# Kernel optimization log

Measured on AMD Instinct MI355X. Metric: run time of the kernel, lower is better.

The kernel has to match this reference:

```python
import jax, jax.numpy as jnp
import numpy as np

B, S, DM, H = 2, 2048, 1024, 16        # dim_model = d_model//2 = 1024
WINDOW, DILATION, N_GLOBAL = 513, 2, 32
HD = DM // H
NEG = -1e9


def build_mask(n, window_size, dilation, global_idx):
    # dilated local window: |i-j| <= (window//2)*dilation and (i-j) % dilation == 0
    i = jnp.arange(n)[:, None]
    j = jnp.arange(n)[None, :]
    d = j - i
    half = window_size // 2
    local = (jnp.abs(d) <= half * dilation) & (jnp.mod(d, dilation) == 0)
    g = jnp.zeros((n,), bool).at[global_idx].set(True)
    # symmetric global token mask: global rows and columns fully attend
    return local | g[:, None] | g[None, :]


def setup_inputs() -> dict:
    key = jax.random.key(0)
    ks = jax.random.split(key, 9)
    std = 0.02
    inp = {
        "q": jax.random.normal(ks[0], (B, S, DM), jnp.float32),
        "k": jax.random.normal(ks[1], (B, S, DM), jnp.float32),
        "v": jax.random.normal(ks[2], (B, S, DM), jnp.float32),
        "Wq": jax.random.normal(ks[3], (DM, DM), jnp.float32) * std,
        "Wk": jax.random.normal(ks[4], (DM, DM), jnp.float32) * std,
        "Wv": jax.random.normal(ks[5], (DM, DM), jnp.float32) * std,
        "Wo": jax.random.normal(ks[6], (DM, DM), jnp.float32) * std,
        "bq": jnp.zeros((DM,), jnp.float32),
        "bk": jnp.zeros((DM,), jnp.float32),
        "bv": jnp.zeros((DM,), jnp.float32),
        "bo": jnp.zeros((DM,), jnp.float32),
        "global_idx": jax.random.randint(ks[7], (N_GLOBAL,), 0, S, jnp.int64)
        if jax.config.jax_enable_x64 else jax.random.randint(ks[7], (N_GLOBAL,), 0, S, jnp.int32),
    }
    return inp


def reference(q, k, v, Wq, Wk, Wv, Wo, bq, bk, bv, bo, global_idx):
    def split(x):  # [B,S,DM] -> [B,H,S,HD]
        return x.reshape(B, S, H, HD).transpose(0, 2, 1, 3)

    qh = split(q @ Wq.T + bq)
    kh = split(k @ Wk.T + bk)
    vh = split(v @ Wv.T + bv)

    scores = jnp.einsum("bhqd,bhkd->bhqk", qh, kh) / jnp.sqrt(jnp.asarray(HD, qh.dtype))
    mask = build_mask(S, WINDOW, DILATION, global_idx)  # [S,S] bool
    scores = jnp.where(mask[None, None], scores, NEG)
    attn = jax.nn.softmax(scores, axis=-1)
    out = jnp.einsum("bhqk,bhkd->bhqd", attn, vh)
    out = out.transpose(0, 2, 1, 3).reshape(B, S, DM)
    return out @ Wo.T + bo
```

## Files before the change

kernel.cpp:

```cpp
#include <hip/hip_runtime.h>
#include <hip/hip_bf16.h>
#include <math.h>

#define BB 2
#define SS 2048
#define DMM 1024
#define HH 16
#define HDD 64
#define NGLOB 32
#define MM 4096
#define SCALE2 0.18033688f

typedef __attribute__((ext_vector_type(8))) short short8;
typedef __attribute__((ext_vector_type(4))) float float4v;

__device__ __forceinline__ short f2bf(float f) {
    union { float f; unsigned u; } x; x.f = f;
    unsigned r = (x.u + 0x7fffu + ((x.u >> 16) & 1u)) >> 16;
    return (short)r;
}

#define ASYNC16(gp, lp) __builtin_amdgcn_global_load_lds( \
    (__attribute__((address_space(1))) void*)(gp), \
    (__attribute__((address_space(3))) void*)(lp), 16, 0, 0)

#define VSL(dim, key) ((dim) * 40 + (((((key) >> 3) ^ (((dim) >> 3) & 3)) << 3) | ((key) & 7)))

__global__ __launch_bounds__(256)
void convert_flat(const float* __restrict__ q, const float* __restrict__ k,
                  const float* __restrict__ v,
                  const float* __restrict__ w0, const float* __restrict__ w1,
                  const float* __restrict__ w2, const float* __restrict__ w3,
                  short* __restrict__ abf, short* __restrict__ wbf,
                  const int* __restrict__ gidx, int* __restrict__ g,
                  int* __restrict__ glist, int* __restrict__ gcount,
                  int* __restrict__ bcnt) {
    int bid = blockIdx.x;
    int t = threadIdx.x;
    if (bid == 6144 + 2048) {
        for (int i = t; i < SS; i += 256) g[i] = 0;
        if (t == 0) *gcount = 0;
        if (t < 32) bcnt[t] = 0;
        __syncthreads();
        if (t < NGLOB) {
            int j = gidx[t];
            if (j >= 0 && j < SS) g[j] = 1;
        }
        __syncthreads();
        for (int j = t; j < SS; j += 256) {
            if (g[j]) {
                int p = atomicAdd(gcount, 1);
                glist[p] = j;
            }
        }
        return;
    }
    const float* src;
    short* dst;
    if (bid < 6144) {
        int z = bid >> 11;
        size_t off = ((size_t)(bid & 2047) << 11) + (size_t)t * 8;
        src = ((z == 0) ? q : (z == 1) ? k : v) + off;
        dst = abf + ((size_t)z << 22) + off;
    } else {
        int y = (bid - 6144) >> 9;
        size_t off = ((size_t)((bid - 6144) & 511) << 11) + (size_t)t * 8;
        src = ((y == 0) ? w0 : (y == 1) ? w1 : (y == 2) ? w2 : w3) + off;
        dst = wbf + ((size_t)y << 20) + off;
    }
    float4 a = *(const float4*)(src);
    float4 b = *(const float4*)(src + 4);
    short8 s;
    s[0]=f2bf(a.x); s[1]=f2bf(a.y); s[2]=f2bf(a.z); s[3]=f2bf(a.w);
    s[4]=f2bf(b.x); s[5]=f2bf(b.y); s[6]=f2bf(b.z); s[7]=f2bf(b.w);
    *(short8*)dst = s;
}

template<int OBF, int HEADSPLIT>
__global__ __launch_bounds__(512, 2)
void gemm256(const short* __restrict__ Abase, const short* __restrict__ Wbase,
             const float* __restrict__ b0, const float* __restrict__ b1,
             const float* __restrict__ b2,
             void* __restrict__ O0p, void* __restrict__ O1p, void* __restrict__ O2p) {
    __shared__ short As[2][256 * 64];
    __shared__ short Ws[2][256 * 64];

    int t = threadIdx.x;
    int z = blockIdx.y;
    const short* A    = Abase + (size_t)z * ((size_t)MM * DMM);
    const short* W    = Wbase + (size_t)z * ((size_t)DMM * DMM);
    const float* bias = (z == 0) ? b0 : (z == 1) ? b1 : b2;
    void* outp        = (z == 0) ? O0p : (z == 1) ? O1p : O2p;

    int bid = blockIdx.x;
    int mt = bid & 15, nt = bid >> 4;
    int m0 = mt * 256, n0 = nt * 256;

    int lane = t & 63, w = t >> 6;
    int quad = lane >> 4, col = lane & 15;
    int wm = (w >> 2) * 128;
    int wn = (w & 3) * 64;

    float4v acc[8][4];
    #pragma unroll
    for (int i = 0; i < 8; i++)
        #pragma unroll
        for (int j = 0; j < 4; j++) acc[i][j] = (float4v){0, 0, 0, 0};

    int srow = t >> 3;
    int scol = ((t & 7) ^ (srow & 7)) * 8;
    const short* Ap = A + (size_t)(m0 + srow) * DMM + scol;
    const short* Wp = W + (size_t)(n0 + srow) * DMM + scol;

    #define ST_W(bf, tt, h) ASYNC16(Wp + (size_t)(h) * 64 * DMM + (size_t)(tt) * 64, \
                                    &Ws[bf][(h) * 4096 + t * 8])
    #define ST_A(bf, tt, h) ASYNC16(Ap + (size_t)(h) * 64 * DMM + (size_t)(tt) * 64, \
                                    &As[bf][(h) * 4096 + t * 8])

    int c7 = col & 7;

    ST_W(0, 0, 0); ST_W(0, 0, 1); ST_W(0, 0, 2); ST_W(0, 0, 3);
    ST_A(0, 0, 0); ST_A(0, 0, 2); ST_A(0, 0, 1); ST_A(0, 0, 3);
    asm volatile("s_waitcnt vmcnt(2)" ::: "memory");
    __builtin_amdgcn_s_barrier();

    for (int it = 0; it < 16; it++) {
        int cur = it & 1, nb = cur ^ 1;
        bool pf = (it < 15);

        short8 bF[4][2];
        #pragma unroll
        for (int j = 0; j < 4; j++) {
            int rB = (wn + 16 * j + col) * 64;
            #pragma unroll
            for (int ks = 0; ks < 2; ks++)
                bF[j][ks] = *(short8*)&Ws[cur][rB + ((((ks << 2) | quad) ^ c7) << 3)];
        }

        #pragma unroll
        for (int p = 0; p < 4; p++) {
            short8 aF[2][2];
            #pragma unroll
            for (int u = 0; u < 2; u++) {
                int rA = (wm + 16 * (2 * p + u) + col) * 64;
                #pragma unroll
                for (int ks = 0; ks < 2; ks++)
                    aF[u][ks] = *(short8*)&As[cur][rA + ((((ks << 2) | quad) ^ c7) << 3)];
            }
            if (pf) {
                if (p == 0)      { ST_W(nb, it + 1, 0); ST_W(nb, it + 1, 1); }
                else if (p == 1) { ST_W(nb, it + 1, 2); ST_W(nb, it + 1, 3); }
                else if (p == 2) { ST_A(nb, it + 1, 0); ST_A(nb, it + 1, 2); }
                else             { ST_A(nb, it + 1, 1); ST_A(nb, it + 1, 3); }
            }
            __builtin_amdgcn_s_barrier();
            __builtin_amdgcn_s_setprio(1);
            #pragma unroll
            for (int ks = 0; ks < 2; ks++)
                #pragma unroll
                for (int u = 0; u < 2; u++)
                    #pragma unroll
                    for (int j = 0; j < 4; j++)
                        acc[2 * p + u][j] = __builtin_amdgcn_mfma_f32_16x16x32_bf16(
                            aF[u][ks], bF[j][ks], acc[2 * p + u][j], 0, 0, 0);
            __builtin_amdgcn_s_setprio(0);
            if (p == 1) {
                if (pf) asm volatile("s_waitcnt vmcnt(4)" ::: "memory");
                else    asm volatile("s_waitcnt vmcnt(0)" ::: "memory");
            }
            if (p == 3 && pf)
                asm volatile("s_waitcnt vmcnt(2)" ::: "memory");
            __builtin_amdgcn_s_barrier();
        }
    }
    #undef ST_W
    #undef ST_A

    #pragma unroll
    for (int i = 0; i < 8; i++) {
        #pragma unroll
        for (int j = 0; j < 4; j++) {
            int n = n0 + wn + 16 * j + col;
            float bn = bias[n];
            #pragma unroll
            for (int r = 0; r < 4; r++) {
                int m = m0 + wm + 16 * i + quad * 4 + r;
                float val = acc[i][j][r] + bn;
                size_t idx;
                if (HEADSPLIT) {
                    int b = m >> 11;
                    int s = m & 2047;
                    int h = n >> 6;
                    int hd = n & 63;
                    idx = (((size_t)b * HH + h) * SS + s) * HDD + hd;
                } else {
                    idx = (size_t)m * DMM + n;
                }
                if (OBF) ((short*)outp)[idx] = f2bf(val);
                else     ((float*)outp)[idx] = val;
            }
        }
    }
}

__global__ __launch_bounds__(512, 2)
void gemm128wo(const short* __restrict__ A, const short* __restrict__ W,
               const float* __restrict__ bias, float* __restrict__ out) {
    __shared__ short As[2][128 * 64];
    __shared__ short Ws[2][128 * 64];

    int t = threadIdx.x;
    int bid = blockIdx.x;
    int mt = bid & 31, nt = bid >> 5;
    int m0 = mt * 128, n0 = nt * 128;

    int lane = t & 63, w = t >> 6;
    int quad = lane >> 4, col = lane & 15;
    int wm = (w >> 2) * 64;
    int wn = (w & 3) * 32;

    float4v acc[4][2];
    #pragma unroll
    for (int i = 0; i < 4; i++)
        #pragma unroll
        for (int j = 0; j < 2; j++) acc[i][j] = (float4v){0, 0, 0, 0};

    int srow = t >> 3;
    int scol = ((t & 7) ^ (srow & 7)) * 8;
    const short* Ap = A + (size_t)(m0 + srow) * DMM + scol;
    const short* Wp = W + (size_t)(n0 + srow) * DMM + scol;

    #define STAGEWO(bf, tt) do { size_t kk = (size_t)(tt) * 64; \
        ASYNC16(Ap + kk,                      &As[bf][t * 8]); \
        ASYNC16(Ap + 64 * (size_t)DMM + kk,   &As[bf][4096 + t * 8]); \
        ASYNC16(Wp + kk,                      &Ws[bf][t * 8]); \
        ASYNC16(Wp + 64 * (size_t)DMM + kk,   &Ws[bf][4096 + t * 8]); \
    } while (0)

    int c7 = col & 7;

    STAGEWO(0, 0);

    for (int it = 0; it < 16; it++) {
        int cur = it & 1;
        if (it < 15) {
            STAGEWO(cur ^ 1, it + 1);
            asm volatile("s_waitcnt vmcnt(4)" ::: "memory");
        } else {
            asm volatile("s_waitcnt vmcnt(0)" ::: "memory");
        }
        __builtin_amdgcn_s_barrier();

        short8 bF[2][2];
        #pragma unroll
        for (int j = 0; j < 2; j++) {
            int rB = (wn + 16 * j + col) * 64;
            #pragma unroll
            for (int ks = 0; ks < 2; ks++)
                bF[j][ks] = *(short8*)&Ws[cur][rB + ((((ks << 2) | quad) ^ c7) << 3)];
        }

        #pragma unroll
        for (int p = 0; p < 2; p++) {
            if (p) __builtin_amdgcn_s_barrier();
            short8 aF[2][2];
            #pragma unroll
            for (int u = 0; u < 2; u++) {
                int rA = (wm + 16 * (2 * p + u) + col) * 64;
                #pragma unroll
                for (int ks = 0; ks < 2; ks++)
                    aF[u][ks] = *(short8*)&As[cur][rA + ((((ks << 2) | quad) ^ c7) << 3)];
            }
            __builtin_amdgcn_s_setprio(1);
            #pragma unroll
            for (int ks = 0; ks < 2; ks++)
                #pragma unroll
                for (int u = 0; u < 2; u++)
                    #pragma unroll
                    for (int j = 0; j < 2; j++)
                        acc[2 * p + u][j] = __builtin_amdgcn_mfma_f32_16x16x32_bf16(
                            aF[u][ks], bF[j][ks], acc[2 * p + u][j], 0, 0, 0);
            __builtin_amdgcn_s_setprio(0);
        }
        __builtin_amdgcn_s_barrier();
    }
    #undef STAGEWO

    #pragma unroll
    for (int i = 0; i < 4; i++) {
        #pragma unroll
        for (int j = 0; j < 2; j++) {
            int n = n0 + wn + 16 * j + col;
            float bn = bias[n];
            #pragma unroll
            for (int r = 0; r < 4; r++) {
                int m = m0 + wm + 16 * i + quad * 4 + r;
                out[(size_t)m * DMM + n] = acc[i][j][r] + bn;
            }
        }
    }
}

__global__ __launch_bounds__(256)
void attn_fused(const short* __restrict__ qh, const short* __restrict__ kh,
                const short* __restrict__ vh, const int* __restrict__ glist,
                const int* __restrict__ gcount, const int* __restrict__ gmap,
                short* __restrict__ ao, float* __restrict__ pl, float* __restrict__ pO,
                int* __restrict__ bcnt) {
    __shared__ __align__(16) char smem[29200];
    int t = threadIdx.x;
    int bid = blockIdx.x;
    int nG = *gcount;

    if (bid < 1024) {
        short* Qs = (short*)smem;
        short* Ks = Qs + 64 * 72;
        short* Vt = Ks + 32 * 72;
        short* Ps = Vt + 64 * 40;
        int*   gjs = (int*)(Ps + 4 * 16 * 40);

        int xcd = bid & 7, idx = bid >> 3;
        int gl  = idx >> 4;
        int qt  = idx & 15;
        int gid = xcd * 8 + gl;
        int z   = gid >> 4;
        int h   = gid & 15;
        int b = z >> 1, p = z & 1;
        int qq0 = qt * 64;

        const short* Qb = qh + ((size_t)(b * HH + h) * SS) * HDD;
        const short* Kb = kh + ((size_t)(b * HH + h) * SS) * HDD;
        const short* Vb = vh + ((size_t)(b * HH + h) * SS) * HDD;

        int row8 = t >> 3;
        int dim8 = (t & 7) * 8;

        #pragma unroll
        for (int rr = 0; rr < 2; rr++) {
            int row = rr * 32 + row8;
            int i = 2 * (qq0 + row) + p;
            short8 qv = *(const short8*)(Qb + (size_t)i * HDD + dim8);
            *(short8*)&Qs[row * 72 + dim8] = qv;
        }
        if (t < 32) gjs[t] = (t < nG) ? glist[t] : -1000000;
        __syncthreads();

        int lane = t & 63, w = t >> 6;
        int quad = lane >> 4, col = lane & 15;

        short8 qf0 = *(short8*)&Qs[(16 * w + col) * 72 + quad * 8];
        short8 qf1 = *(short8*)&Qs[(16 * w + col) * 72 + 32 + quad * 8];

        float4v O0 = {0,0,0,0}, O1 = {0,0,0,0}, O2 = {0,0,0,0}, O3 = {0,0,0,0};
        float lst[4] = {0.f, 0.f, 0.f, 0.f};

        short8 kvP, vvP, kvN, vvN;
        {
            int srow = 2 * (qq0 - 256 + row8) + p;
            srow = srow < 0 ? 0 : (srow > SS - 1 ? SS - 1 : srow);
            kvP = *(const short8*)(Kb + (size_t)srow * HDD + dim8);
            vvP = *(const short8*)(Vb + (size_t)srow * HDD + dim8);
        }

        for (int c = 0; c < 19; c++) {
            __syncthreads();
            *(short8*)&Ks[row8 * 72 + dim8] = kvP;
            #pragma unroll
            for (int j = 0; j < 8; j++) {
                int d = dim8 + j;
                Vt[VSL(d, row8)] = vvP[j];
            }
            if (c < 18) {
                int cn = c + 1;
                int ch0n = qq0 - 256 + cn * 32;
                int srow;
                if (cn < 18) srow = 2 * (ch0n + row8) + p;
                else         srow = (row8 < nG) ? gjs[row8] : 0;
                srow = srow < 0 ? 0 : (srow > SS - 1 ? SS - 1 : srow);
                kvN = *(const short8*)(Kb + (size_t)srow * HDD + dim8);
                vvN = *(const short8*)(Vb + (size_t)srow * HDD + dim8);
            }
            __syncthreads();

            int ch0 = qq0 - 256 + c * 32;

            short8 kA0 = *(short8*)&Ks[col * 72 + quad * 8];
            short8 kA1 = *(short8*)&Ks[col * 72 + 32 + quad * 8];
            short8 kB0 = *(short8*)&Ks[(16 + col) * 72 + quad * 8];
            short8 kB1 = *(short8*)&Ks[(16 + col) * 72 + 32 + quad * 8];
            float4v sA = {0,0,0,0}, sB = {0,0,0,0};
            sA = __builtin_amdgcn_mfma_f32_16x16x32_bf16(qf0, kA0, sA, 0, 0, 0);
            sA = __builtin_amdgcn_mfma_f32_16x16x32_bf16(qf1, kA1, sA, 0, 0, 0);
            sB = __builtin_amdgcn_mfma_f32_16x16x32_bf16(qf0, kB0, sB, 0, 0, 0);
            sB = __builtin_amdgcn_mfma_f32_16x16x32_bf16(qf1, kB1, sB, 0, 0, 0);

            if (c < 18) {
                int nlo = -ch0;
                int nhi = 1023 - ch0;
                #pragma unroll
                for (int r = 0; r < 4; r++) {
                    int qq = qq0 + 16 * w + quad * 4 + r;
                    int u  = qq - ch0;
                    int lo = max(u - 256, nlo);
                    int hi = min(u + 256, nhi);
                    bool vA = (col >= lo) && (col <= hi);
                    bool vB = (col + 16 >= lo) && (col + 16 <= hi);
                    float pa = vA ? exp2f(sA[r] * SCALE2) : 0.f;
                    float pb = vB ? exp2f(sB[r] * SCALE2) : 0.f;
                    lst[r] += pa + pb;
                    Ps[(w * 16 + quad * 4 + r) * 40 + col]      = f2bf(pa);
                    Ps[(w * 16 + quad * 4 + r) * 40 + col + 16] = f2bf(pb);
                }
            } else {
                #pragma unroll
                for (int r = 0; r < 4; r++) {
                    int qq = qq0 + 16 * w + quad * 4 + r;
                    int i = 2 * qq + p;
                    int jA = gjs[col], jB = gjs[col + 16];
                    int dA = jA - i, dB = jB - i;
                    int aA = dA < 0 ? -dA : dA;
                    int aB = dB < 0 ? -dB : dB;
                    bool vA = (jA >= 0) && !((aA <= 512) && ((dA & 1) == 0));
                    bool vB = (jB >= 0) && !((aB <= 512) && ((dB & 1) == 0));
                    float pa = vA ? exp2f(sA[r] * SCALE2) : 0.f;
                    float pb = vB ? exp2f(sB[r] * SCALE2) : 0.f;
                    lst[r] += pa + pb;
                    Ps[(w * 16 + quad * 4 + r) * 40 + col]      = f2bf(pa);
                    Ps[(w * 16 + quad * 4 + r) * 40 + col + 16] = f2bf(pb);
                }
            }
            asm volatile("s_waitcnt lgkmcnt(0)" ::: "memory");

            short8 pf  = *(short8*)&Ps[(w * 16 + col) * 40 + quad * 8];
            short8 vf0 = *(short8*)&Vt[(col) * 40 + ((quad ^ ((col >> 3) & 3)) << 3)];
            short8 vf1 = *(short8*)&Vt[(16 + col) * 40 + ((quad ^ (((16 + col) >> 3) & 3)) << 3)];
            short8 vf2 = *(short8*)&Vt[(32 + col) * 40 + ((quad ^ (((32 + col) >> 3) & 3)) << 3)];
            short8 vf3 = *(short8*)&Vt[(48 + col) * 40 + ((quad ^ (((48 + col) >> 3) & 3)) << 3)];
            O0 = __builtin_amdgcn_mfma_f32_16x16x32_bf16(pf, vf0, O0, 0, 0, 0);
            O1 = __builtin_amdgcn_mfma_f32_16x16x32_bf16(pf, vf1, O1, 0, 0, 0);
            O2 = __builtin_amdgcn_mfma_f32_16x16x32_bf16(pf, vf2, O2, 0, 0, 0);
            O3 = __builtin_amdgcn_mfma_f32_16x16x32_bf16(pf, vf3, O3, 0, 0, 0);

            kvP = kvN; vvP = vvN;
        }

        #pragma unroll
        for (int r = 0; r < 4; r++) {
            float l = lst[r];
            #pragma unroll
            for (int mk = 1; mk < 16; mk <<= 1) l += __shfl_xor(l, mk);
            float inv = 1.0f / l;
            int q = 16 * w + quad * 4 + r;
            int i = 2 * (qq0 + q) + p;
            if (!gmap[i]) {
                short* dst = ao + ((size_t)b * SS + i) * DMM + h * HDD;
                dst[col]      = f2bf(O0[r] * inv);
                dst[col + 16] = f2bf(O1[r] * inv);
                dst[col + 32] = f2bf(O2[r] * inv);
                dst[col + 48] = f2bf(O3[r] * inv);
            }
        }
    } else {
        short* Qs  = (short*)smem;
        short* Ksf = Qs + 32 * 72;
        short* Vtf = Ksf + 2 * 32 * 72;
        short* Ps  = Vtf + 2 * 64 * 40;
        int* sflag = (int*)(smem + 29184);

        int r0 = bid - 1024;
        int s = r0 & 7, h = (r0 >> 3) & 15, b = r0 >> 7;

        const short* Qb = qh + ((size_t)(b * HH + h) * SS) * HDD;
        const short* Kb = kh + ((size_t)(b * HH + h) * SS) * HDD;
        const short* Vb = vh + ((size_t)(b * HH + h) * SS) * HDD;

        int row8 = t >> 3, dim8 = (t & 7) * 8;
        {
            int cq = row8 < nG ? row8 : 0;
            int src = glist[cq];
            short8 qv = *(const short8*)(Qb + (size_t)src * HDD + dim8);
            *(short8*)&Qs[row8 * 72 + dim8] = qv;
        }
        __syncthreads();

        int lane = t & 63, w = t >> 6;
        int quad = lane >> 4, col = lane & 15;
        int g = w >> 1, qt = w & 1;

        short8 qf0 = *(short8*)&Qs[(qt * 16 + col) * 72 + quad * 8];
        short8 qf1 = *(short8*)&Qs[(qt * 16 + col) * 72 + 32 + quad * 8];

        float4v O0 = {0,0,0,0}, O1 = {0,0,0,0}, O2 = {0,0,0,0}, O3 = {0,0,0,0};
        float lst[4] = {0.f, 0.f, 0.f, 0.f};

        int js0 = s * 256;
        for (int it = 0; it < 4; it++) {
            __syncthreads();
            int r64 = t >> 2, dimb = (t & 3) * 16;
            int j = js0 + it * 64 + r64;
            const short* kp = Kb + (size_t)j * HDD + dimb;
            const short* vp = Vb + (size_t)j * HDD + dimb;
            short8 k0 = *(const short8*)kp, k1 = *(const short8*)(kp + 8);
            short8 v0 = *(const short8*)vp, v1 = *(const short8*)(vp + 8);
            int half = r64 >> 5, r32 = r64 & 31;
            short* Ksh = Ksf + half * (32 * 72);
            short* Vth = Vtf + half * (64 * 40);
            *(short8*)&Ksh[r32 * 72 + dimb]     = k0;
            *(short8*)&Ksh[r32 * 72 + dimb + 8] = k1;
            #pragma unroll
            for (int u = 0; u < 8; u++) {
                int d = dimb + u;
                Vth[VSL(d, r32)] = v0[u];
            }
            #pragma unroll
            for (int u = 0; u < 8; u++) {
                int d = dimb + 8 + u;
                Vth[VSL(d, r32)] = v1[u];
            }
            __syncthreads();

            short* Ksg = Ksf + g * (32 * 72);
            short* Vtg = Vtf + g * (64 * 40);
            short8 kA0 = *(short8*)&Ksg[col * 72 + quad * 8];
            short8 kA1 = *(short8*)&Ksg[col * 72 + 32 + quad * 8];
            short8 kB0 = *(short8*)&Ksg[(16 + col) * 72 + quad * 8];
            short8 kB1 = *(short8*)&Ksg[(16 + col) * 72 + 32 + quad * 8];
            float4v sA = {0,0,0,0}, sB = {0,0,0,0};
            sA = __builtin_amdgcn_mfma_f32_16x16x32_bf16(qf0, kA0, sA, 0, 0, 0);
            sA = __builtin_amdgcn_mfma_f32_16x16x32_bf16(qf1, kA1, sA, 0, 0, 0);
            sB = __builtin_amdgcn_mfma_f32_16x16x32_bf16(qf0, kB0, sB, 0, 0, 0);
            sB = __builtin_amdgcn_mfma_f32_16x16x32_bf16(qf1, kB1, sB, 0, 0, 0);

            #pragma unroll
            for (int r = 0; r < 4; r++) {
                float pa = exp2f(sA[r] * SCALE2);
                float pb = exp2f(sB[r] * SCALE2);
                lst[r] += pa + pb;
                Ps[(w * 16 + quad * 4 + r) * 40 + col]      = f2bf(pa);
                Ps[(w * 16 + quad * 4 + r) * 40 + col + 16] = f2bf(pb);
            }
            asm volatile("s_waitcnt lgkmcnt(0)" ::: "memory");

            short8 pf  = *(short8*)&Ps[(w * 16 + col) * 40 + quad * 8];
            short8 vf0 = *(short8*)&Vtg[(col) * 40 + ((quad ^ ((col >> 3) & 3)) << 3)];
            short8 vf1 = *(short8*)&Vtg[(16 + col) * 40 + ((quad ^ (((16 + col) >> 3) & 3)) << 3)];
            short8 vf2 = *(short8*)&Vtg[(32 + col) * 40 + ((quad ^ (((32 + col) >> 3) & 3)) << 3)];
            short8 vf3 = *(short8*)&Vtg[(48 + col) * 40 + ((quad ^ (((48 + col) >> 3) & 3)) << 3)];
            O0 = __builtin_amdgcn_mfma_f32_16x16x32_bf16(pf, vf0, O0, 0, 0, 0);
            O1 = __builtin_amdgcn_mfma_f32_16x16x32_bf16(pf, vf1, O1, 0, 0, 0);
            O2 = __builtin_amdgcn_mfma_f32_16x16x32_bf16(pf, vf2, O2, 0, 0, 0);
            O3 = __builtin_amdgcn_mfma_f32_16x16x32_bf16(pf, vf3, O3, 0, 0, 0);
        }

        int sp = s * 2 + g;
        size_t base = ((size_t)(b * HH + h) * 16 + sp) * 32;
        #pragma unroll
        for (int r = 0; r < 4; r++) {
            float l = lst[r];
            #pragma unroll
            for (int mk = 1; mk < 16; mk <<= 1) l += __shfl_xor(l, mk);
            int q = qt * 16 + quad * 4 + r;
            if (col == 0) pl[base + q] = l;
            float* Od = pO + (base + q) * 64;
            Od[col]      = O0[r];
            Od[col + 16] = O1[r];
            Od[col + 32] = O2[r];
            Od[col + 48] = O3[r];
        }

        __threadfence();
        __syncthreads();
        if (t == 0) {
            int bh = b * HH + h;
            *sflag = atomicAdd(&bcnt[bh], 1);
        }
        __syncthreads();
        if (*sflag == 7) {
            __threadfence();
            int d = t & 63, qg = t >> 6;
            size_t bh2 = ((size_t)(b * HH + h) * 16) * 32;
            for (int q2 = qg; q2 < nG; q2 += 4) {
                float L = 0.f, acc2 = 0.f;
                #pragma unroll
                for (int sp2 = 0; sp2 < 16; sp2++) {
                    L    += pl[bh2 + sp2 * 32 + q2];
                    acc2 += pO[(bh2 + sp2 * 32 + q2) * 64 + d];
                }
                int i = glist[q2];
                ao[((size_t)b * SS + i) * DMM + h * HDD + d] = f2bf(acc2 / L);
            }
        }
    }
}

extern "C" void kernel_launch(void* const* d_in, const int* in_sizes, int n_in,
                              void* d_out, int out_size, void* d_ws, size_t ws_size,
                              hipStream_t stream) {
    const float* q  = (const float*)d_in[0];
    const float* k  = (const float*)d_in[1];
    const float* v  = (const float*)d_in[2];
    const float* Wq = (const float*)d_in[3];
    const float* Wk = (const float*)d_in[4];
    const float* Wv = (const float*)d_in[5];
    const float* Wo = (const float*)d_in[6];
    const float* bq = (const float*)d_in[7];
    const float* bk = (const float*)d_in[8];
    const float* bv = (const float*)d_in[9];
    const float* bo = (const float*)d_in[10];
    const int* gidx = (const int*)d_in[11];
    float* out = (float*)d_out;

    const size_t NE = (size_t)BB * SS * DMM;
    const size_t WE = (size_t)DMM * DMM;
    int*   g      = (int*)d_ws;
    int*   glist  = g + SS;
    int*   gcount = glist + SS;
    int*   bcnt   = gcount + 1;
    short* qh     = (short*)((char*)d_ws + 32768);
    short* kh     = qh + NE;
    short* vh     = kh + NE;
    short* ao     = vh + NE;
    short* wbf    = ao + NE;
    short* wo     = wbf + 3 * WE;
    short* abf    = wbf + 4 * WE;
    float* pl     = (float*)abf;
    float* pO     = pl + 16384;

    convert_flat<<<8193, 256, 0, stream>>>(q, k, v, Wq, Wk, Wv, Wo, abf, wbf,
                                           gidx, g, glist, gcount, bcnt);

    dim3 gq(64, 3);
    gemm256<1, 1><<<gq, 512, 0, stream>>>(abf, wbf, bq, bk, bv, qh, kh, vh);

    attn_fused<<<1280, 256, 0, stream>>>(qh, kh, vh, glist, gcount, g, ao, pl, pO, bcnt);

    gemm128wo<<<256, 512, 0, stream>>>(ao, wo, bo, out);
}
```

Measured before the change: 254.8 us.

## Process global-row attention in one block per head, dropping split-K cross-block reduction

Global-query attention blocks previously split the 2048 keys across 8 blocks per (batch, head), wrote partial O and l to global scratch, and used an atomic counter with threadfences so the last block could reduce. Now one block per (batch, head) loops over all 32 key chunks, and its two wave groups combine their partials through shared memory before writing the normalized output. This removes the global partial traffic, atomics and fences, but each global block now does 8x more serial work, which may lengthen the tail of the attention kernel.

Result: faster. 226.4 us (-11.2%).

```diff
diff --git a/kernel.cpp b/kernel.cpp
--- a/kernel.cpp
+++ b/kernel.cpp
@@ -33,14 +33,12 @@
                   const float* __restrict__ w2, const float* __restrict__ w3,
                   short* __restrict__ abf, short* __restrict__ wbf,
                   const int* __restrict__ gidx, int* __restrict__ g,
-                  int* __restrict__ glist, int* __restrict__ gcount,
-                  int* __restrict__ bcnt) {
+                  int* __restrict__ glist, int* __restrict__ gcount) {
     int bid = blockIdx.x;
     int t = threadIdx.x;
     if (bid == 6144 + 2048) {
         for (int i = t; i < SS; i += 256) g[i] = 0;
         if (t == 0) *gcount = 0;
-        if (t < 32) bcnt[t] = 0;
         __syncthreads();
         if (t < NGLOB) {
             int j = gidx[t];
@@ -305,8 +303,7 @@
 void attn_fused(const short* __restrict__ qh, const short* __restrict__ kh,
                 const short* __restrict__ vh, const int* __restrict__ glist,
                 const int* __restrict__ gcount, const int* __restrict__ gmap,
-                short* __restrict__ ao, float* __restrict__ pl, float* __restrict__ pO,
-                int* __restrict__ bcnt) {
+                short* __restrict__ ao) {
     __shared__ __align__(16) char smem[29200];
     int t = threadIdx.x;
     int bid = blockIdx.x;
@@ -465,10 +462,9 @@
         short* Ksf = Qs + 32 * 72;
         short* Vtf = Ksf + 2 * 32 * 72;
         short* Ps  = Vtf + 2 * 64 * 40;
-        int* sflag = (int*)(smem + 29184);
 
         int r0 = bid - 1024;
-        int s = r0 & 7, h = (r0 >> 3) & 15, b = r0 >> 7;
+        int h = r0 & 15, b = r0 >> 4;
 
         const short* Qb = qh + ((size_t)(b * HH + h) * SS) * HDD;
         const short* Kb = kh + ((size_t)(b * HH + h) * SS) * HDD;
@@ -493,11 +489,10 @@
         float4v O0 = {0,0,0,0}, O1 = {0,0,0,0}, O2 = {0,0,0,0}, O3 = {0,0,0,0};
         float lst[4] = {0.f, 0.f, 0.f, 0.f};
 
-        int js0 = s * 256;
-        for (int it = 0; it < 4; it++) {
+        for (int chunk = 0; chunk < 32; chunk++) {
             __syncthreads();
             int r64 = t >> 2, dimb = (t & 3) * 16;
-            int j = js0 + it * 64 + r64;
+            int j = chunk * 64 + r64;
             const short* kp = Kb + (size_t)j * HDD + dimb;
             const short* vp = Vb + (size_t)j * HDD + dimb;
             short8 k0 = *(const short8*)kp, k1 = *(const short8*)(kp + 8);
@@ -552,42 +547,43 @@
             O3 = __builtin_amdgcn_mfma_f32_16x16x32_bf16(pf, vf3, O3, 0, 0, 0);
         }
 
-        int sp = s * 2 + g;
-        size_t base = ((size_t)(b * HH + h) * 16 + sp) * 32;
+        float lred[4];
         #pragma unroll
         for (int r = 0; r < 4; r++) {
             float l = lst[r];
             #pragma unroll
             for (int mk = 1; mk < 16; mk <<= 1) l += __shfl_xor(l, mk);
-            int q = qt * 16 + quad * 4 + r;
-            if (col == 0) pl[base + q] = l;
-            float* Od = pO + (base + q) * 64;
-            Od[col]      = O0[r];
-            Od[col + 16] = O1[r];
-            Od[col + 32] = O2[r];
-            Od[col + 48] = O3[r];
-        }
-
-        __threadfence();
+            lred[r] = l;
+        }
         __syncthreads();
-        if (t == 0) {
-            int bh = b * HH + h;
-            *sflag = atomicAdd(&bcnt[bh], 1);
+        float* comb = (float*)smem;
+        if (g == 1) {
+            float* dstL = comb + ((qt << 6) + lane) * 20;
+            #pragma unroll
+            for (int r = 0; r < 4; r++) {
+                dstL[r]      = O0[r];
+                dstL[4 + r]  = O1[r];
+                dstL[8 + r]  = O2[r];
+                dstL[12 + r] = O3[r];
+                dstL[16 + r] = lred[r];
+            }
         }
         __syncthreads();
-        if (*sflag == 7) {
-            __threadfence();
-            int d = t & 63, qg = t >> 6;
-            size_t bh2 = ((size_t)(b * HH + h) * 16) * 32;
-            for (int q2 = qg; q2 < nG; q2 += 4) {
-                float L = 0.f, acc2 = 0.f;
-                #pragma unroll
-                for (int sp2 = 0; sp2 < 16; sp2++) {
-                    L    += pl[bh2 + sp2 * 32 + q2];
-                    acc2 += pO[(bh2 + sp2 * 32 + q2) * 64 + d];
+        if (g == 0) {
+            float* srcL = comb + ((qt << 6) + lane) * 20;
+            #pragma unroll
+            for (int r = 0; r < 4; r++) {
+                int q = qt * 16 + quad * 4 + r;
+                if (q < nG) {
+                    float L = lred[r] + srcL[16 + r];
+                    float inv = 1.0f / L;
+                    int i = glist[q];
+                    short* dst = ao + ((size_t)b * SS + i) * DMM + h * HDD;
+                    dst[col]      = f2bf((O0[r] + srcL[r])      * inv);
+                    dst[col + 16] = f2bf((O1[r] + srcL[4 + r])  * inv);
+                    dst[col + 32] = f2bf((O2[r] + srcL[8 + r])  * inv);
+                    dst[col + 48] = f2bf((O3[r] + srcL[12 + r]) * inv);
                 }
-                int i = glist[q2];
-                ao[((size_t)b * SS + i) * DMM + h * HDD + d] = f2bf(acc2 / L);
             }
         }
     }
@@ -615,7 +611,6 @@
     int*   g      = (int*)d_ws;
     int*   glist  = g + SS;
     int*   gcount = glist + SS;
-    int*   bcnt   = gcount + 1;
     short* qh     = (short*)((char*)d_ws + 32768);
     short* kh     = qh + NE;
     short* vh     = kh + NE;
@@ -623,16 +618,14 @@
     short* wbf    = ao + NE;
     short* wo     = wbf + 3 * WE;
     short* abf    = wbf + 4 * WE;
-    float* pl     = (float*)abf;
-    float* pO     = pl + 16384;
 
     convert_flat<<<8193, 256, 0, stream>>>(q, k, v, Wq, Wk, Wv, Wo, abf, wbf,
-                                           gidx, g, glist, gcount, bcnt);
+                                           gidx, g, glist, gcount);
 
     dim3 gq(64, 3);
     gemm256<1, 1><<<gq, 512, 0, stream>>>(abf, wbf, bq, bk, bv, qh, kh, vh);
 
-    attn_fused<<<1280, 256, 0, stream>>>(qh, kh, vh, glist, gcount, g, ao, pl, pO, bcnt);
+    attn_fused<<<1056, 256, 0, stream>>>(qh, kh, vh, glist, gcount, g, ao);
 
     gemm128wo<<<256, 512, 0, stream>>>(ao, wo, bo, out);
 }
```
